# Optimization experiments

Measured on AMD Instinct MI355X. Metric: run time of the kernel, lower is better.

## Reference

```python
import jax, jax.numpy as jnp
import numpy as np

N_QUBITS = 8
DIM = 2 ** N_QUBITS  # 256 state-vector dim
EMBED = 512
FFN = 2048
B, S = 4, 8192


def setup_inputs() -> dict:
    key = jax.random.key(0)
    k_x, k_w1, k_b1, k_w2, k_b2 = jax.random.split(key, 5)
    # Random-layer unitary: QR of a complex Gaussian matrix (Haar-like).
    rng = np.random.default_rng(0)
    A = rng.standard_normal((DIM, DIM)) + 1j * rng.standard_normal((DIM, DIM))
    Q, _ = np.linalg.qr(A)
    U_re = jnp.asarray(Q.real, dtype=jnp.float32)
    U_im = jnp.asarray(Q.imag, dtype=jnp.float32)
    x = jax.random.normal(k_x, (B, S, EMBED), dtype=jnp.float32)
    # torch nn.Linear params: y = x @ W.T + b
    W1 = jax.random.normal(k_w1, (FFN, N_QUBITS), dtype=jnp.float32) / np.sqrt(N_QUBITS)
    b1 = jax.random.normal(k_b1, (FFN,), dtype=jnp.float32) * 0.01
    W2 = jax.random.normal(k_w2, (EMBED, FFN), dtype=jnp.float32) / np.sqrt(FFN)
    b2 = jax.random.normal(k_b2, (EMBED,), dtype=jnp.float32) * 0.01
    return {"x": x, "U_re": U_re, "U_im": U_im, "W1": W1, "b1": b1, "W2": W2, "b2": b2}


def _pauliz_expectations(U_re, U_im, n_qubits):
    # Device starts in |0...0>, so post-layer state is column 0 of U.
    psi_re = U_re[:, 0]
    psi_im = U_im[:, 0]
    probs = psi_re * psi_re + psi_im * psi_im            # [2^n]
    p = probs.reshape((2,) * n_qubits)                   # wire i -> axis i
    zs = []
    for i in range(n_qubits):
        pm = jnp.moveaxis(p, i, 0).reshape(2, -1).sum(axis=-1)
        zs.append(pm[0] - pm[1])                         # <Z_i> = P(0) - P(1)
    return jnp.stack(zs)                                 # [n_qubits]


def reference(x, U_re, U_im, W1, b1, W2, b2):
    b, s, _ = x.shape
    n_qubits = W1.shape[1]
    z = _pauliz_expectations(U_re, U_im, n_qubits)       # identical for every token
    feat = jnp.broadcast_to(z, (b, s, n_qubits))         # [B, S, n_qubits]
    # dropout is identity at inference
    h = jax.nn.relu(jnp.einsum('bsq,fq->bsf', feat, W1) + b1)
    out = jnp.einsum('bsf,ef->bse', h, W2) + b2          # [B, S, embed]
    return out
```

## Files before the change

### kernel.cpp

```cpp
#include <hip/hip_runtime.h>

#define DIM   256
#define NQ    8
#define EMBED 512
#define FFN   2048
#define ROWS  (4 * 8192)
#define OUT_ELEMS (ROWS * EMBED)
#define OUT_VEC4  (EMBED / 4)
#define OUT_TOTAL4 (OUT_ELEMS / 4)

__global__ void k_ov(const float* __restrict__ U_re,
                     const float* __restrict__ U_im,
                     const float* __restrict__ W1,
                     const float* __restrict__ b1,
                     const float* __restrict__ W2,
                     const float* __restrict__ b2,
                     float* __restrict__ ov) {
    int t = threadIdx.x;
    int e = blockIdx.x;

    float re = U_re[t * DIM];
    float im = U_im[t * DIM];
    float p  = re * re + im * im;

    float zp[NQ];
#pragma unroll
    for (int q = 0; q < NQ; ++q)
        zp[q] = ((t >> (NQ - 1 - q)) & 1) ? -p : p;
#pragma unroll
    for (int off = 32; off > 0; off >>= 1) {
#pragma unroll
        for (int q = 0; q < NQ; ++q)
            zp[q] += __shfl_down(zp[q], off, 64);
    }
    __shared__ float zw[4][NQ];
    if ((t & 63) == 0) {
#pragma unroll
        for (int q = 0; q < NQ; ++q) zw[t >> 6][q] = zp[q];
    }
    __syncthreads();
    __shared__ float zs[NQ];
    if (t < NQ) zs[t] = zw[0][t] + zw[1][t] + zw[2][t] + zw[3][t];
    __syncthreads();

    float zr[NQ];
#pragma unroll
    for (int q = 0; q < NQ; ++q) zr[q] = zs[q];

    __shared__ float h[FFN];
#pragma unroll
    for (int r = 0; r < FFN / 256; ++r) {
        int f = r * 256 + t;
        const float4* w = (const float4*)(W1 + f * NQ);
        float4 w0 = w[0], w1 = w[1];
        float acc = b1[f];
        acc += zr[0] * w0.x + zr[1] * w0.y + zr[2] * w0.z + zr[3] * w0.w;
        acc += zr[4] * w1.x + zr[5] * w1.y + zr[6] * w1.z + zr[7] * w1.w;
        h[f] = fmaxf(acc, 0.f);
    }
    __syncthreads();

    const float4* row = (const float4*)(W2 + (size_t)e * FFN);
    const float4* h4  = (const float4*)h;
    float4 a0 = row[t],       hb0 = h4[t];
    float4 a1 = row[256 + t], hb1 = h4[256 + t];
    float acc = a0.x * hb0.x + a0.y * hb0.y + a0.z * hb0.z + a0.w * hb0.w
              + a1.x * hb1.x + a1.y * hb1.y + a1.z * hb1.z + a1.w * hb1.w;
#pragma unroll
    for (int off = 32; off > 0; off >>= 1)
        acc += __shfl_down(acc, off, 64);
    __shared__ float wsum[4];
    if ((t & 63) == 0) wsum[t >> 6] = acc;
    __syncthreads();
    if (t == 0)
        ov[e] = wsum[0] + wsum[1] + wsum[2] + wsum[3] + b2[e];
}

__global__ void k_broadcast(const float* __restrict__ ov,
                            float* __restrict__ out) {
    const float4* ov4 = (const float4*)ov;
    float4* out4 = (float4*)out;
    int idx = blockIdx.x * blockDim.x + threadIdx.x;
    int stride = gridDim.x * blockDim.x;
    float4 v = ov4[idx & (OUT_VEC4 - 1)];
    for (; idx < OUT_TOTAL4; idx += stride)
        out4[idx] = v;
}

extern "C" void kernel_launch(void* const* d_in, const int* in_sizes, int n_in,
                              void* d_out, int out_size, void* d_ws, size_t ws_size,
                              hipStream_t stream) {
    const float* U_re = (const float*)d_in[1];
    const float* U_im = (const float*)d_in[2];
    const float* W1   = (const float*)d_in[3];
    const float* b1   = (const float*)d_in[4];
    const float* W2   = (const float*)d_in[5];
    const float* b2   = (const float*)d_in[6];
    float* out = (float*)d_out;

    float* ov = (float*)d_ws;

    k_ov       <<<EMBED, 256, 0, stream>>>(U_re, U_im, W1, b1, W2, b2, ov);
    k_broadcast<<<4096,  256, 0, stream>>>(ov, out);
}
```

Baseline: 120.8 us.

## Fuse output-vector computation and broadcast into one tiled kernel

Merges the two kernels into a single launch in which each block recomputes the Pauli-Z features and hidden activations. It then computes a 32-wide slice of the output vector and writes that slice across a tile of 1024 rows. This removes the second launch, the workspace round trip and the serialization between stages. In exchange, the small front computation is repeated in every block, W2 reads grow several-fold (served mostly from cache), and stores become 128-byte strided segments instead of fully contiguous lines.

```diff
diff --git a/kernel.cpp b/kernel.cpp
--- a/kernel.cpp
+++ b/kernel.cpp
@@ -5,19 +5,24 @@
 #define EMBED 512
 #define FFN   2048
 #define ROWS  (4 * 8192)
-#define OUT_ELEMS (ROWS * EMBED)
 #define OUT_VEC4  (EMBED / 4)
-#define OUT_TOTAL4 (OUT_ELEMS / 4)
+#define W_DIMS 32
+#define CT_N   (EMBED / W_DIMS)
+#define R_ROWS 1024
+#define RT_N   (ROWS / R_ROWS)
+#define GRID   (CT_N * RT_N)
 
-__global__ void k_ov(const float* __restrict__ U_re,
-                     const float* __restrict__ U_im,
-                     const float* __restrict__ W1,
-                     const float* __restrict__ b1,
-                     const float* __restrict__ W2,
-                     const float* __restrict__ b2,
-                     float* __restrict__ ov) {
-    int t = threadIdx.x;
-    int e = blockIdx.x;
+__global__ void __launch_bounds__(256)
+k_fused(const float* __restrict__ U_re,
+        const float* __restrict__ U_im,
+        const float* __restrict__ W1,
+        const float* __restrict__ b1,
+        const float* __restrict__ W2,
+        const float* __restrict__ b2,
+        float* __restrict__ out) {
+    int t  = threadIdx.x;
+    int ct = blockIdx.x & (CT_N - 1);
+    int rt = blockIdx.x >> 4;
 
     float re = U_re[t * DIM];
     float im = U_im[t * DIM];
@@ -60,31 +65,36 @@
     }
     __syncthreads();
 
-    const float4* row = (const float4*)(W2 + (size_t)e * FFN);
-    const float4* h4  = (const float4*)h;
-    float4 a0 = row[t],       hb0 = h4[t];
-    float4 a1 = row[256 + t], hb1 = h4[256 + t];
-    float acc = a0.x * hb0.x + a0.y * hb0.y + a0.z * hb0.z + a0.w * hb0.w
-              + a1.x * hb1.x + a1.y * hb1.y + a1.z * hb1.z + a1.w * hb1.w;
+    __shared__ float ovs[W_DIMS];
+    const float4* h4 = (const float4*)h;
+    int wave = t >> 6, lane = t & 63;
 #pragma unroll
-    for (int off = 32; off > 0; off >>= 1)
-        acc += __shfl_down(acc, off, 64);
-    __shared__ float wsum[4];
-    if ((t & 63) == 0) wsum[t >> 6] = acc;
+    for (int pss = 0; pss < W_DIMS / 4; ++pss) {
+        int d = pss * 4 + wave;
+        int e = ct * W_DIMS + d;
+        const float4* row = (const float4*)(W2 + (size_t)e * FFN);
+        float acc = 0.f;
+#pragma unroll
+        for (int j = 0; j < 8; ++j) {
+            float4 a = row[j * 64 + lane];
+            float4 b = h4[j * 64 + lane];
+            acc += a.x * b.x + a.y * b.y + a.z * b.z + a.w * b.w;
+        }
+#pragma unroll
+        for (int off = 32; off > 0; off >>= 1)
+            acc += __shfl_down(acc, off, 64);
+        if (lane == 0) ovs[d] = acc + b2[e];
+    }
     __syncthreads();
-    if (t == 0)
-        ov[e] = wsum[0] + wsum[1] + wsum[2] + wsum[3] + b2[e];
-}
 
-__global__ void k_broadcast(const float* __restrict__ ov,
-                            float* __restrict__ out) {
-    const float4* ov4 = (const float4*)ov;
+    const float4* ovs4 = (const float4*)ovs;
+    float4 v = ovs4[t & 7];
     float4* out4 = (float4*)out;
-    int idx = blockIdx.x * blockDim.x + threadIdx.x;
-    int stride = gridDim.x * blockDim.x;
-    float4 v = ov4[idx & (OUT_VEC4 - 1)];
-    for (; idx < OUT_TOTAL4; idx += stride)
-        out4[idx] = v;
+    int rr = t >> 3;
+    size_t base = (size_t)rt * R_ROWS * OUT_VEC4 + ct * 8 + (t & 7);
+#pragma unroll
+    for (int i = 0; i < R_ROWS / 32; ++i)
+        out4[base + (size_t)(rr + i * 32) * OUT_VEC4] = v;
 }
 
 extern "C" void kernel_launch(void* const* d_in, const int* in_sizes, int n_in,
@@ -98,8 +108,5 @@
     const float* b2   = (const float*)d_in[6];
     float* out = (float*)d_out;
 
-    float* ov = (float*)d_ws;
-
-    k_ov       <<<EMBED, 256, 0, stream>>>(U_re, U_im, W1, b1, W2, b2, ov);
-    k_broadcast<<<4096,  256, 0, stream>>>(ov, out);
+    k_fused<<<GRID, 256, 0, stream>>>(U_re, U_im, W1, b1, W2, b2, out);
 }
```

New measurement: 123.7 us. 2.4% more time.
